# Kernel tuning notes

Measured on AMD Instinct MI355X. Metric: run time of the kernel, lower is better.

## Reference

```python
import jax, jax.numpy as jnp
import numpy as np

B, S, D, H = 2, 2048, 1024, 16
HD = D // H

def setup_inputs() -> dict:
    key = jax.random.key(0)
    ks = jax.random.split(key, 9)
    scale = 1.0 / np.sqrt(D)
    return {
        "query": jax.random.normal(ks[0], (B, S, D), jnp.float32),
        "key":   jax.random.normal(ks[1], (B, S, D), jnp.float32),
        "value": jax.random.normal(ks[2], (B, S, D), jnp.float32),
        "Wq_w": jax.random.normal(ks[3], (D, D), jnp.float32) * scale,
        "Wq_b": jax.random.normal(ks[4], (D,), jnp.float32) * scale,
        "Wk_w": jax.random.normal(ks[5], (D, D), jnp.float32) * scale,
        "Wk_b": jax.random.normal(ks[6], (D,), jnp.float32) * scale,
        "Wv_w": jax.random.normal(ks[7], (D, D), jnp.float32) * scale,
        "Wv_b": jax.random.normal(ks[8], (D,), jnp.float32) * scale,
    }

def reference(query, key, value, Wq_w, Wq_b, Wk_w, Wk_b, Wv_w, Wv_b):
    b, s, d = query.shape
    # torch Linear: y = x @ W.T + b
    Q = query @ Wq_w.T + Wq_b
    K = key   @ Wk_w.T + Wk_b
    V = value @ Wv_w.T + Wv_b
    # [B, H, S, HD]
    Q = Q.reshape(b, -1, H, HD).transpose(0, 2, 1, 3)
    K = K.reshape(b, -1, H, HD).transpose(0, 2, 1, 3)
    V = V.reshape(b, -1, H, HD).transpose(0, 2, 1, 3)
    scores = jnp.einsum("bhqd,bhkd->bhqk", Q, K) / jnp.sqrt(jnp.float32(HD))
    attn = jax.nn.softmax(scores, axis=-1)
    context = jnp.einsum("bhqk,bhkd->bhqd", attn, V)  # [B,H,S,HD]
    attn_output = context.transpose(0, 2, 1, 3).reshape(b, -1, H * HD)  # [B,S,D]
    return (context, attn_output)
```

## Files before the change

### kernel.cpp

```cpp
#include <hip/hip_runtime.h>
#include <hip/hip_bf16.h>

constexpr int Bb = 2, Ss = 2048, Dd = 1024, Hh = 16, HD = 64;
constexpr int Mrows = Bb * Ss;
constexpr float QSCALE = 0.125f * 1.44269504088896f;
constexpr size_t CTX_ELEMS = (size_t)Bb * Hh * Ss * HD;

typedef __attribute__((ext_vector_type(8)))  short        short8;
typedef __attribute__((ext_vector_type(4)))  float        floatx4;
typedef __attribute__((ext_vector_type(16))) float        floatx16;
typedef __attribute__((ext_vector_type(4)))  unsigned int uintx4;
typedef __attribute__((ext_vector_type(8)))  __bf16       bf16x8;

#define DEVI __device__ __forceinline__

DEVI unsigned short f2bf(float f) {
  union { float f; unsigned u; } x; x.f = f;
  return (unsigned short)((x.u + 0x7fffu + ((x.u >> 16) & 1u)) >> 16);
}
DEVI float fexp2(float x) {
#if __has_builtin(__builtin_amdgcn_exp2f)
  return __builtin_amdgcn_exp2f(x);
#else
  return __expf(x * 0.6931471805599453f);
#endif
}

constexpr size_t XE = (size_t)Mrows * Dd;
constexpr size_t WE = (size_t)Dd * Dd;
constexpr size_t OFF_W = 3 * XE;
constexpr size_t OFF_O = 3 * XE + 3 * WE;
constexpr size_t WS_NEED = (OFF_O + 3 * XE) * 2;

__global__ __launch_bounds__(256) void convert_bf16(
    const float* __restrict__ q, const float* __restrict__ k, const float* __restrict__ v,
    const float* __restrict__ wq, const float* __restrict__ wk, const float* __restrict__ wv,
    unsigned short* __restrict__ dst)
{
  const int sel = blockIdx.y;
  const float* src; size_t n, off;
  switch (sel) {
    case 0:  src = q;  n = XE; off = 0;            break;
    case 1:  src = k;  n = XE; off = XE;           break;
    case 2:  src = v;  n = XE; off = 2 * XE;       break;
    case 3:  src = wq; n = WE; off = OFF_W;        break;
    case 4:  src = wk; n = WE; off = OFF_W + WE;   break;
    default: src = wv; n = WE; off = OFF_W + 2*WE; break;
  }
  unsigned short* d = dst + off;
  const size_t stride = (size_t)gridDim.x * blockDim.x;
  for (size_t i = (size_t)blockIdx.x * blockDim.x + threadIdx.x; i < n / 8; i += stride) {
    const floatx4 a = *(const floatx4*)(src + i * 8);
    const floatx4 b = *(const floatx4*)(src + i * 8 + 4);
    short8 o;
    #pragma unroll
    for (int j = 0; j < 4; ++j) { o[j] = (short)f2bf(a[j]); o[4 + j] = (short)f2bf(b[j]); }
    *(short8*)(d + i * 8) = o;
  }
}

template<bool SWAP>
DEVI void store_out(floatx4 (&acc)[4][4], const float* __restrict__ bias,
                    unsigned short* __restrict__ out, float oscale,
                    int bm, int bn, int wm, int wn, int lrow, int lg)
{
  if constexpr (!SWAP) {
    #pragma unroll
    for (int ni = 0; ni < 4; ++ni) {
      const int gcol = bn * 128 + wn + ni * 16 + lrow;
      const float bval = bias[gcol];
      const int h = gcol >> 6, hd = gcol & 63;
      #pragma unroll
      for (int mi = 0; mi < 4; ++mi)
        #pragma unroll
        for (int r = 0; r < 4; ++r) {
          const int grow = bm * 128 + wm + mi * 16 + lg * 4 + r;
          const int b = grow >> 11, s = grow & 2047;
          out[(((size_t)(b * Hh + h) * Ss + s) << 6) + hd] = f2bf((acc[mi][ni][r] + bval) * oscale);
        }
    }
  } else {
    #pragma unroll
    for (int ni = 0; ni < 4; ++ni)
      #pragma unroll
      for (int r = 0; r < 4; ++r) {
        const int n = bn * 128 + wn + ni * 16 + lg * 4 + r;
        const float bval = bias[n];
        #pragma unroll
        for (int mi = 0; mi < 4; ++mi) {
          const int m = bm * 128 + wm + mi * 16 + lrow;
          out[(size_t)n * Mrows + m] = f2bf(acc[mi][ni][r] + bval);
        }
      }
  }
}

DEVI void gload16(const unsigned short* g, unsigned short* l) {
  __builtin_amdgcn_global_load_lds(
      (const __attribute__((address_space(1))) unsigned int*)g,
      (__attribute__((address_space(3))) unsigned int*)l, 16, 0, 0);
}

template<bool SWAP>
DEVI void gemm_core_bf16(const unsigned short* __restrict__ X,
                         const unsigned short* __restrict__ W,
                         const float* __restrict__ bias,
                         unsigned short* __restrict__ out, float oscale,
                         unsigned short* As, unsigned short* Bs, int bm, int bn)
{
  const int t = threadIdx.x, wid = t >> 6, lane = t & 63;
  const int lrow = lane & 15, lg = lane >> 4;
  const int wm = (wid >> 1) * 64, wn = (wid & 1) * 64;

  const int srow = lane >> 3;
  const int gch  = (lane & 7) ^ srow;
  const unsigned short* gA = X + (size_t)(bm * 128 + wid * 32 + srow) * Dd + gch * 8;
  const unsigned short* gB = W + (size_t)(bn * 128 + wid * 32 + srow) * Dd + gch * 8;
  unsigned short* lA = As + wid * 4 * 512;
  unsigned short* lB = Bs + wid * 4 * 512;

  floatx4 acc[4][4];
  #pragma unroll
  for (int i = 0; i < 4; ++i)
    #pragma unroll
    for (int j = 0; j < 4; ++j) acc[i][j] = 0.0f;

  for (int k0 = 0; k0 < Dd; k0 += 64) {
    __syncthreads();
    #pragma unroll
    for (int j = 0; j < 4; ++j) {
      gload16(gA + (size_t)j * 8 * Dd + k0, lA + j * 512);
      gload16(gB + (size_t)j * 8 * Dd + k0, lB + j * 512);
    }
    __syncthreads();

    #pragma unroll
    for (int kf = 0; kf < 2; ++kf) {
      bf16x8 af[4], bf[4];
      #pragma unroll
      for (int mi = 0; mi < 4; ++mi) {
        const int row = wm + mi * 16 + lrow;
        const int ch  = ((kf << 2) | lg) ^ (lrow & 7);
        af[mi] = __builtin_bit_cast(bf16x8, *(const short8*)&As[row * 64 + (ch << 3)]);
      }
      #pragma unroll
      for (int ni = 0; ni < 4; ++ni) {
        const int row = wn + ni * 16 + lrow;
        const int ch  = ((kf << 2) | lg) ^ (lrow & 7);
        bf[ni] = __builtin_bit_cast(bf16x8, *(const short8*)&Bs[row * 64 + (ch << 3)]);
      }
      #pragma unroll
      for (int mi = 0; mi < 4; ++mi)
        #pragma unroll
        for (int ni = 0; ni < 4; ++ni) {
          if constexpr (SWAP)
            acc[mi][ni] = __builtin_amdgcn_mfma_f32_16x16x32_bf16(bf[ni], af[mi], acc[mi][ni], 0, 0, 0);
          else
            acc[mi][ni] = __builtin_amdgcn_mfma_f32_16x16x32_bf16(af[mi], bf[ni], acc[mi][ni], 0, 0, 0);
        }
    }
  }
  store_out<SWAP>(acc, bias, out, oscale, bm, bn, wm, wn, lrow, lg);
}

__global__ __launch_bounds__(256, 3) void qkv_gemm_bf16(
    const unsigned short* __restrict__ ws,
    const float* __restrict__ bq, const float* __restrict__ bk, const float* __restrict__ bv,
    unsigned short* __restrict__ outbase)
{
  __shared__ __align__(16) unsigned short As[128 * 64];
  __shared__ __align__(16) unsigned short Bs[128 * 64];

  const int id  = blockIdx.y * 256 + blockIdx.x;
  const int swz = (id & 7) * 96 + (id >> 3);
  const int sel = swz >> 8;
  const int bx  = swz & 255;
  const int bm = bx >> 3, bn = bx & 7;

  const unsigned short* X = ws + (size_t)sel * XE;
  const unsigned short* W = ws + OFF_W + (size_t)sel * WE;
  const float* bias = sel == 0 ? bq : sel == 1 ? bk : bv;
  unsigned short* out = outbase + (size_t)sel * XE;

  if (sel == 2) gemm_core_bf16<true >(X, W, bias, out, 1.0f,   As, Bs, bm, bn);
  else          gemm_core_bf16<false>(X, W, bias, out, sel == 0 ? QSCALE : 1.0f, As, Bs, bm, bn);
}

constexpr int APAD = 40;

template<bool SWAP>
DEVI void gemm_core_f32(const float* __restrict__ X, const float* __restrict__ W,
                        const float* __restrict__ bias, unsigned short* __restrict__ out,
                        float oscale, unsigned short* As, unsigned short* Bs, int bm, int bn)
{
  const int t = threadIdx.x, wid = t >> 6, lane = t & 63;
  const int lrow = lane & 15, lg = lane >> 4;
  const int wm = (wid >> 1) * 64, wn = (wid & 1) * 64;

  floatx4 acc[4][4];
  #pragma unroll
  for (int i = 0; i < 4; ++i)
    #pragma unroll
    for (int j = 0; j < 4; ++j) acc[i][j] = 0.0f;

  for (int k0 = 0; k0 < Dd; k0 += 32) {
    __syncthreads();
    #pragma unroll
    for (int half = 0; half < 2; ++half) {
      const int cidx = t + half * 256;
      const int r = cidx >> 2, c = cidx & 3;
      {
        const float* ga = X + (size_t)(bm * 128 + r) * Dd + k0 + c * 8;
        const floatx4 x0 = *(const floatx4*)ga;
        const floatx4 x1 = *(const floatx4*)(ga + 4);
        short8 va;
        #pragma unroll
        for (int j = 0; j < 4; ++j) { va[j] = (short)f2bf(x0[j]); va[4+j] = (short)f2bf(x1[j]); }
        *(short8*)&As[r * APAD + c * 8] = va;
      }
      {
        const float* gb = W + (size_t)(bn * 128 + r) * Dd + k0 + c * 8;
        const floatx4 x0 = *(const floatx4*)gb;
        const floatx4 x1 = *(const floatx4*)(gb + 4);
        short8 vb;
        #pragma unroll
        for (int j = 0; j < 4; ++j) { vb[j] = (short)f2bf(x0[j]); vb[4+j] = (short)f2bf(x1[j]); }
        *(short8*)&Bs[r * APAD + c * 8] = vb;
      }
    }
    __syncthreads();

    bf16x8 af[4], bf[4];
    #pragma unroll
    for (int mi = 0; mi < 4; ++mi)
      af[mi] = __builtin_bit_cast(bf16x8, *(const short8*)&As[(wm + mi * 16 + lrow) * APAD + lg * 8]);
    #pragma unroll
    for (int ni = 0; ni < 4; ++ni)
      bf[ni] = __builtin_bit_cast(bf16x8, *(const short8*)&Bs[(wn + ni * 16 + lrow) * APAD + lg * 8]);

    #pragma unroll
    for (int mi = 0; mi < 4; ++mi)
      #pragma unroll
      for (int ni = 0; ni < 4; ++ni) {
        if constexpr (SWAP)
          acc[mi][ni] = __builtin_amdgcn_mfma_f32_16x16x32_bf16(bf[ni], af[mi], acc[mi][ni], 0, 0, 0);
        else
          acc[mi][ni] = __builtin_amdgcn_mfma_f32_16x16x32_bf16(af[mi], bf[ni], acc[mi][ni], 0, 0, 0);
      }
  }
  store_out<SWAP>(acc, bias, out, oscale, bm, bn, wm, wn, lrow, lg);
}

__global__ __launch_bounds__(256, 2) void qkv_gemm_f32(
    const float* __restrict__ q, const float* __restrict__ k, const float* __restrict__ v,
    const float* __restrict__ wq, const float* __restrict__ wk, const float* __restrict__ wv,
    const float* __restrict__ bq, const float* __restrict__ bk, const float* __restrict__ bv,
    unsigned short* __restrict__ outbase)
{
  __shared__ __align__(16) unsigned short As[128 * APAD];
  __shared__ __align__(16) unsigned short Bs[128 * APAD];

  const int id  = blockIdx.y * 256 + blockIdx.x;
  const int swz = (id & 7) * 96 + (id >> 3);
  const int sel = swz >> 8;
  const int bx  = swz & 255;
  const int bm = bx >> 3, bn = bx & 7;

  const float* X = sel == 0 ? q : sel == 1 ? k : v;
  const float* W = sel == 0 ? wq : sel == 1 ? wk : wv;
  const float* bias = sel == 0 ? bq : sel == 1 ? bk : bv;
  unsigned short* out = outbase + (size_t)sel * XE;

  if (sel == 2) gemm_core_f32<true >(X, W, bias, out, 1.0f, As, Bs, bm, bn);
  else          gemm_core_f32<false>(X, W, bias, out, sel == 0 ? QSCALE : 1.0f, As, Bs, bm, bn);
}

__global__ __launch_bounds__(256, 2) void attn_fwd(
    const unsigned short* __restrict__ Qw, const unsigned short* __restrict__ Kw,
    const unsigned short* __restrict__ Vw, float* __restrict__ out)
{
  __shared__ __align__(16) unsigned short Ks[2][64 * 64];
  __shared__ __align__(16) unsigned short Vt[2][64 * 64];

  const int id  = blockIdx.y * 16 + blockIdx.x;
  const int swz = (id & 7) * 64 + (id >> 3);
  const int qb  = swz & 15, bh = swz >> 4;
  const int b   = bh >> 4, h = bh & 15;

  const int t = threadIdx.x, wid = t >> 6, lane = t & 63;
  const int l31 = lane & 31, hi = lane >> 5;
  const unsigned short* Qb = Qw + (size_t)bh * (Ss * HD);
  const unsigned short* Kb = Kw + (size_t)bh * (Ss * HD);
  const unsigned short* Vg = Vw + (size_t)(h * 64) * Mrows + b * Ss;
  const int q0 = qb * 128 + wid * 32;

  bf16x8 qf[4];
  #pragma unroll
  for (int hs = 0; hs < 4; ++hs)
    qf[hs] = __builtin_bit_cast(bf16x8,
        *(const short8*)(Qb + (size_t)(q0 + l31) * 64 + hs * 16 + hi * 8));

  floatx16 ctx[2], lsum;
  #pragma unroll
  for (int nb = 0; nb < 2; ++nb) ctx[nb] = 0.0f;
  lsum = 0.0f;

  short8 ones_s;
  #pragma unroll
  for (int j = 0; j < 8; ++j) ones_s[j] = (short)0x3F80;
  const bf16x8 ones = __builtin_bit_cast(bf16x8, ones_s);

  const int rl = lane >> 3;
  const int cs = (lane & 7) ^ rl;
  auto stage = [&](int kv0, int buf) {
    #pragma unroll
    for (int i = 0; i < 2; ++i) {
      const int row = wid * 16 + i * 8 + rl;
      gload16(Kb + (size_t)(kv0 + row) * 64 + cs * 8, &Ks[buf][(wid * 16 + i * 8) * 64]);
      gload16(Vg + (size_t)row * Mrows + kv0 + cs * 8, &Vt[buf][(wid * 16 + i * 8) * 64]);
    }
  };

  stage(0, 0);

  for (int it = 0; it < Ss / 64; ++it) {
    const int cur = it & 1;
    __syncthreads();
    if (it + 1 < Ss / 64) stage((it + 1) * 64, cur ^ 1);

    floatx16 s[2];
    s[0] = 0.0f; s[1] = 0.0f;
    __builtin_amdgcn_s_setprio(1);
    #pragma unroll
    for (int kvb = 0; kvb < 2; ++kvb)
      #pragma unroll
      for (int hs = 0; hs < 4; ++hs) {
        const int ch = ((hs << 1) | hi) ^ (l31 & 7);
        const bf16x8 kf = __builtin_bit_cast(bf16x8,
            *(const short8*)&Ks[cur][(kvb * 32 + l31) * 64 + (ch << 3)]);
        s[kvb] = __builtin_amdgcn_mfma_f32_32x32x16_bf16(kf, qf[hs], s[kvb], 0, 0, 0);
      }
    __builtin_amdgcn_s_setprio(0);

    #pragma unroll
    for (int kvb = 0; kvb < 2; ++kvb) {
      float p[16];
      #pragma unroll
      for (int r = 0; r < 16; ++r) p[r] = fexp2(s[kvb][r]);
      unsigned int c[8];
      #pragma unroll
      for (int i = 0; i < 8; ++i)
        asm("v_cvt_pk_bf16_f32 %0, %1, %2" : "=v"(c[i]) : "v"(p[2 * i]), "v"(p[2 * i + 1]));

      #pragma unroll
      for (int ks2 = 0; ks2 < 2; ++ks2) {
        unsigned int w0 = c[4 * ks2 + 0], w2 = c[4 * ks2 + 2];
        unsigned int w1 = c[4 * ks2 + 1], w3 = c[4 * ks2 + 3];
        asm("v_permlane32_swap_b32 %0, %1" : "+v"(w0), "+v"(w2));
        asm("v_permlane32_swap_b32 %0, %1" : "+v"(w1), "+v"(w3));
        uintx4 paw; paw[0] = w0; paw[1] = w1; paw[2] = w2; paw[3] = w3;
        const bf16x8 pa = __builtin_bit_cast(bf16x8, paw);

        const int ks = kvb * 2 + ks2;
        __builtin_amdgcn_s_setprio(1);
        lsum = __builtin_amdgcn_mfma_f32_32x32x16_bf16(pa, ones, lsum, 0, 0, 0);
        #pragma unroll
        for (int nb = 0; nb < 2; ++nb) {
          const int ch = ((ks << 1) | hi) ^ (l31 & 7);
          const bf16x8 vf = __builtin_bit_cast(bf16x8,
              *(const short8*)&Vt[cur][(nb * 32 + l31) * 64 + (ch << 3)]);
          ctx[nb] = __builtin_amdgcn_mfma_f32_32x32x16_bf16(pa, vf, ctx[nb], 0, 0, 0);
        }
        __builtin_amdgcn_s_setprio(0);
      }
    }
  }

  #pragma unroll
  for (int r = 0; r < 16; ++r) {
    const float inv = 1.0f / lsum[r];
    const int qrow = q0 + (r & 3) + 8 * (r >> 2) + 4 * hi;
    #pragma unroll
    for (int nb = 0; nb < 2; ++nb) {
      const int hd = nb * 32 + l31;
      const float val = ctx[nb][r] * inv;
      out[((size_t)bh * Ss + qrow) * 64 + hd] = val;
      out[CTX_ELEMS + (((size_t)(b * Ss + qrow)) << 10) + (h << 6) + hd] = val;
    }
  }
}

extern "C" void kernel_launch(void* const* d_in, const int* in_sizes, int n_in,
                              void* d_out, int out_size, void* d_ws, size_t ws_size,
                              hipStream_t stream) {
  const float* q  = (const float*)d_in[0];
  const float* k  = (const float*)d_in[1];
  const float* v  = (const float*)d_in[2];
  const float* wq = (const float*)d_in[3];
  const float* bq = (const float*)d_in[4];
  const float* wk = (const float*)d_in[5];
  const float* bk = (const float*)d_in[6];
  const float* wv = (const float*)d_in[7];
  const float* bv = (const float*)d_in[8];
  unsigned short* ws = (unsigned short*)d_ws;
  float* out = (float*)d_out;

  if (ws_size >= WS_NEED) {
    convert_bf16<<<dim3(256, 6), 256, 0, stream>>>(q, k, v, wq, wk, wv, ws);
    qkv_gemm_bf16<<<dim3(256, 3), 256, 0, stream>>>(ws, bq, bk, bv, ws + OFF_O);
    attn_fwd<<<dim3(16, 32), 256, 0, stream>>>(ws + OFF_O, ws + OFF_O + XE, ws + OFF_O + 2 * XE, out);
  } else {
    qkv_gemm_f32<<<dim3(256, 3), 256, 0, stream>>>(q, k, v, wq, wk, wv, bq, bk, bv, ws);
    attn_fwd<<<dim3(16, 32), 256, 0, stream>>>(ws, ws + XE, ws + 2 * XE, out);
  }
}
```

Before: 92.97 us.

## Load K/V tiles directly from global into registers, dropping LDS staging

New measurement: 164.2 us. 76.6% more time.

```diff
diff --git a/kernel.cpp b/kernel.cpp
--- a/kernel.cpp
+++ b/kernel.cpp
@@ -275,13 +275,12 @@
   else          gemm_core_f32<false>(X, W, bias, out, sel == 0 ? QSCALE : 1.0f, As, Bs, bm, bn);
 }
 
+constexpr int NT = Ss / 64;
+
 __global__ __launch_bounds__(256, 2) void attn_fwd(
     const unsigned short* __restrict__ Qw, const unsigned short* __restrict__ Kw,
     const unsigned short* __restrict__ Vw, float* __restrict__ out)
 {
-  __shared__ __align__(16) unsigned short Ks[2][64 * 64];
-  __shared__ __align__(16) unsigned short Vt[2][64 * 64];
-
   const int id  = blockIdx.y * 16 + blockIdx.x;
   const int swz = (id & 7) * 64 + (id >> 3);
   const int qb  = swz & 15, bh = swz >> 4;
@@ -289,10 +288,11 @@
 
   const int t = threadIdx.x, wid = t >> 6, lane = t & 63;
   const int l31 = lane & 31, hi = lane >> 5;
-  const unsigned short* Qb = Qw + (size_t)bh * (Ss * HD);
-  const unsigned short* Kb = Kw + (size_t)bh * (Ss * HD);
-  const unsigned short* Vg = Vw + (size_t)(h * 64) * Mrows + b * Ss;
   const int q0 = qb * 128 + wid * 32;
+
+  const unsigned short* Qb  = Qw + (size_t)bh * (Ss * HD);
+  const unsigned short* KbL = Kw + (size_t)bh * (Ss * HD) + (size_t)l31 * 64 + hi * 8;
+  const unsigned short* VbL = Vw + (size_t)(h * 64 + l31) * Mrows + b * Ss + hi * 8;
 
   bf16x8 qf[4];
   #pragma unroll
@@ -301,32 +301,36 @@
         *(const short8*)(Qb + (size_t)(q0 + l31) * 64 + hs * 16 + hi * 8));
 
   floatx16 ctx[2], lsum;
-  #pragma unroll
-  for (int nb = 0; nb < 2; ++nb) ctx[nb] = 0.0f;
-  lsum = 0.0f;
+  ctx[0] = 0.0f; ctx[1] = 0.0f; lsum = 0.0f;
 
   short8 ones_s;
   #pragma unroll
   for (int j = 0; j < 8; ++j) ones_s[j] = (short)0x3F80;
   const bf16x8 ones = __builtin_bit_cast(bf16x8, ones_s);
 
-  const int rl = lane >> 3;
-  const int cs = (lane & 7) ^ rl;
-  auto stage = [&](int kv0, int buf) {
-    #pragma unroll
-    for (int i = 0; i < 2; ++i) {
-      const int row = wid * 16 + i * 8 + rl;
-      gload16(Kb + (size_t)(kv0 + row) * 64 + cs * 8, &Ks[buf][(wid * 16 + i * 8) * 64]);
-      gload16(Vg + (size_t)row * Mrows + kv0 + cs * 8, &Vt[buf][(wid * 16 + i * 8) * 64]);
-    }
+  auto loadK = [&](bf16x8 (&kd)[8], int kv0) {
+    #pragma unroll
+    for (int kvb = 0; kvb < 2; ++kvb)
+      #pragma unroll
+      for (int hs = 0; hs < 4; ++hs)
+        kd[kvb * 4 + hs] = __builtin_bit_cast(bf16x8,
+            *(const short8*)(KbL + (size_t)(kv0 + kvb * 32) * 64 + hs * 16));
   };
-
-  stage(0, 0);
-
-  for (int it = 0; it < Ss / 64; ++it) {
-    const int cur = it & 1;
-    __syncthreads();
-    if (it + 1 < Ss / 64) stage((it + 1) * 64, cur ^ 1);
+  auto loadV = [&](bf16x8 (&vd)[8], int kv0) {
+    #pragma unroll
+    for (int nb = 0; nb < 2; ++nb)
+      #pragma unroll
+      for (int ks = 0; ks < 4; ++ks)
+        vd[nb * 4 + ks] = __builtin_bit_cast(bf16x8,
+            *(const short8*)(VbL + (size_t)(nb * 32) * Mrows + kv0 + ks * 16));
+  };
+
+  auto tile = [&](bf16x8 (&kc)[8], bf16x8 (&kn)[8], int it) {
+    const int kv0 = it * 64;
+    bf16x8 vb[8];
+    loadV(vb, kv0);
+    const int kvn = (it + 1 < NT) ? kv0 + 64 : 0;
+    loadK(kn, kvn);
 
     floatx16 s[2];
     s[0] = 0.0f; s[1] = 0.0f;
@@ -334,12 +338,8 @@
     #pragma unroll
     for (int kvb = 0; kvb < 2; ++kvb)
       #pragma unroll
-      for (int hs = 0; hs < 4; ++hs) {
-        const int ch = ((hs << 1) | hi) ^ (l31 & 7);
-        const bf16x8 kf = __builtin_bit_cast(bf16x8,
-            *(const short8*)&Ks[cur][(kvb * 32 + l31) * 64 + (ch << 3)]);
-        s[kvb] = __builtin_amdgcn_mfma_f32_32x32x16_bf16(kf, qf[hs], s[kvb], 0, 0, 0);
-      }
+      for (int hs = 0; hs < 4; ++hs)
+        s[kvb] = __builtin_amdgcn_mfma_f32_32x32x16_bf16(kc[kvb * 4 + hs], qf[hs], s[kvb], 0, 0, 0);
     __builtin_amdgcn_s_setprio(0);
 
     #pragma unroll
@@ -364,16 +364,18 @@
         const int ks = kvb * 2 + ks2;
         __builtin_amdgcn_s_setprio(1);
         lsum = __builtin_amdgcn_mfma_f32_32x32x16_bf16(pa, ones, lsum, 0, 0, 0);
-        #pragma unroll
-        for (int nb = 0; nb < 2; ++nb) {
-          const int ch = ((ks << 1) | hi) ^ (l31 & 7);
-          const bf16x8 vf = __builtin_bit_cast(bf16x8,
-              *(const short8*)&Vt[cur][(nb * 32 + l31) * 64 + (ch << 3)]);
-          ctx[nb] = __builtin_amdgcn_mfma_f32_32x32x16_bf16(pa, vf, ctx[nb], 0, 0, 0);
-        }
+        ctx[0] = __builtin_amdgcn_mfma_f32_32x32x16_bf16(pa, vb[ks],     ctx[0], 0, 0, 0);
+        ctx[1] = __builtin_amdgcn_mfma_f32_32x32x16_bf16(pa, vb[4 + ks], ctx[1], 0, 0, 0);
         __builtin_amdgcn_s_setprio(0);
       }
     }
+  };
+
+  bf16x8 kA[8], kB[8];
+  loadK(kA, 0);
+  for (int it = 0; it < NT; it += 2) {
+    tile(kA, kB, it);
+    tile(kB, kA, it + 1);
   }
 
   #pragma unroll
```

## Software-pipeline attention loop to overlap next tile's QK softmax with current PV

Applied to the files above, without the earlier changes.

Measured after the change: 93.28 us. Within noise of the previous version (+0.3%).

```diff
diff --git a/kernel.cpp b/kernel.cpp
--- a/kernel.cpp
+++ b/kernel.cpp
@@ -275,6 +275,8 @@
   else          gemm_core_f32<false>(X, W, bias, out, sel == 0 ? QSCALE : 1.0f, As, Bs, bm, bn);
 }
 
+constexpr int NT = Ss / 64;
+
 __global__ __launch_bounds__(256, 2) void attn_fwd(
     const unsigned short* __restrict__ Qw, const unsigned short* __restrict__ Kw,
     const unsigned short* __restrict__ Vw, float* __restrict__ out)
@@ -301,9 +303,7 @@
         *(const short8*)(Qb + (size_t)(q0 + l31) * 64 + hs * 16 + hi * 8));
 
   floatx16 ctx[2], lsum;
-  #pragma unroll
-  for (int nb = 0; nb < 2; ++nb) ctx[nb] = 0.0f;
-  lsum = 0.0f;
+  ctx[0] = 0.0f; ctx[1] = 0.0f; lsum = 0.0f;
 
   short8 ones_s;
   #pragma unroll
@@ -312,7 +312,8 @@
 
   const int rl = lane >> 3;
   const int cs = (lane & 7) ^ rl;
-  auto stage = [&](int kv0, int buf) {
+  auto stage = [&](int T) {
+    const int kv0 = T * 64, buf = T & 1;
     #pragma unroll
     for (int i = 0; i < 2; ++i) {
       const int row = wid * 16 + i * 8 + rl;
@@ -321,13 +322,8 @@
     }
   };
 
-  stage(0, 0);
-
-  for (int it = 0; it < Ss / 64; ++it) {
-    const int cur = it & 1;
-    __syncthreads();
-    if (it + 1 < Ss / 64) stage((it + 1) * 64, cur ^ 1);
-
+  auto qk_soft = [&](int T, uintx4 (&pa)[4]) {
+    const int cur = T & 1;
     floatx16 s[2];
     s[0] = 0.0f; s[1] = 0.0f;
     __builtin_amdgcn_s_setprio(1);
@@ -351,7 +347,6 @@
       #pragma unroll
       for (int i = 0; i < 8; ++i)
         asm("v_cvt_pk_bf16_f32 %0, %1, %2" : "=v"(c[i]) : "v"(p[2 * i]), "v"(p[2 * i + 1]));
-
       #pragma unroll
       for (int ks2 = 0; ks2 < 2; ++ks2) {
         unsigned int w0 = c[4 * ks2 + 0], w2 = c[4 * ks2 + 2];
@@ -359,21 +354,46 @@
         asm("v_permlane32_swap_b32 %0, %1" : "+v"(w0), "+v"(w2));
         asm("v_permlane32_swap_b32 %0, %1" : "+v"(w1), "+v"(w3));
         uintx4 paw; paw[0] = w0; paw[1] = w1; paw[2] = w2; paw[3] = w3;
-        const bf16x8 pa = __builtin_bit_cast(bf16x8, paw);
-
-        const int ks = kvb * 2 + ks2;
-        __builtin_amdgcn_s_setprio(1);
-        lsum = __builtin_amdgcn_mfma_f32_32x32x16_bf16(pa, ones, lsum, 0, 0, 0);
-        #pragma unroll
-        for (int nb = 0; nb < 2; ++nb) {
-          const int ch = ((ks << 1) | hi) ^ (l31 & 7);
-          const bf16x8 vf = __builtin_bit_cast(bf16x8,
-              *(const short8*)&Vt[cur][(nb * 32 + l31) * 64 + (ch << 3)]);
-          ctx[nb] = __builtin_amdgcn_mfma_f32_32x32x16_bf16(pa, vf, ctx[nb], 0, 0, 0);
-        }
-        __builtin_amdgcn_s_setprio(0);
-      }
-    }
+        pa[kvb * 2 + ks2] = paw;
+      }
+    }
+  };
+
+  auto body = [&](int t_, uintx4 (&paC)[4], uintx4 (&paN)[4]) {
+    const int cur = t_ & 1;
+    bf16x8 vb[8];
+    #pragma unroll
+    for (int nb = 0; nb < 2; ++nb)
+      #pragma unroll
+      for (int ks = 0; ks < 4; ++ks) {
+        const int ch = ((ks << 1) | hi) ^ (l31 & 7);
+        vb[nb * 4 + ks] = __builtin_bit_cast(bf16x8,
+            *(const short8*)&Vt[cur][(nb * 32 + l31) * 64 + (ch << 3)]);
+      }
+    __syncthreads();
+    if (t_ + 2 < NT) stage(t_ + 2);
+    if (t_ + 1 < NT) qk_soft(t_ + 1, paN);
+
+    __builtin_amdgcn_s_setprio(1);
+    #pragma unroll
+    for (int ks = 0; ks < 4; ++ks) {
+      const bf16x8 pab = __builtin_bit_cast(bf16x8, paC[ks]);
+      lsum   = __builtin_amdgcn_mfma_f32_32x32x16_bf16(pab, ones,       lsum,   0, 0, 0);
+      ctx[0] = __builtin_amdgcn_mfma_f32_32x32x16_bf16(pab, vb[ks],     ctx[0], 0, 0, 0);
+      ctx[1] = __builtin_amdgcn_mfma_f32_32x32x16_bf16(pab, vb[4 + ks], ctx[1], 0, 0, 0);
+    }
+    __builtin_amdgcn_s_setprio(0);
+  };
+
+  stage(0);
+  stage(1);
+  __syncthreads();
+  uintx4 paA[4], paB[4];
+  qk_soft(0, paA);
+
+  for (int it = 0; it < NT; it += 2) {
+    body(it,     paA, paB);
+    body(it + 1, paB, paA);
   }
 
   #pragma unroll
```

## Split attention KV range in halves with combine kernel, replace MFMA row-sum

Applied to the files above, without the earlier changes.

New measurement: 100.6 us. 8.2% more time.

```diff
diff --git a/kernel.cpp b/kernel.cpp
--- a/kernel.cpp
+++ b/kernel.cpp
@@ -31,6 +31,9 @@
 constexpr size_t OFF_W = 3 * XE;
 constexpr size_t OFF_O = 3 * XE + 3 * WE;
 constexpr size_t WS_NEED = (OFF_O + 3 * XE) * 2;
+constexpr size_t P0_E = 0;
+constexpr size_t LA_E = 8388608;
+constexpr size_t LB_E = 8912896;
 
 __global__ __launch_bounds__(256) void convert_bf16(
     const float* __restrict__ q, const float* __restrict__ k, const float* __restrict__ v,
@@ -275,17 +278,32 @@
   else          gemm_core_f32<false>(X, W, bias, out, sel == 0 ? QSCALE : 1.0f, As, Bs, bm, bn);
 }
 
-__global__ __launch_bounds__(256, 2) void attn_fwd(
+template<bool SPLIT>
+__global__ __launch_bounds__(256, 4) void attn_fwd(
     const unsigned short* __restrict__ Qw, const unsigned short* __restrict__ Kw,
-    const unsigned short* __restrict__ Vw, float* __restrict__ out)
+    const unsigned short* __restrict__ Vw,
+    float* __restrict__ p0, float* __restrict__ la,
+    float* __restrict__ p1, float* __restrict__ lb,
+    float* __restrict__ out)
 {
   __shared__ __align__(16) unsigned short Ks[2][64 * 64];
   __shared__ __align__(16) unsigned short Vt[2][64 * 64];
-
-  const int id  = blockIdx.y * 16 + blockIdx.x;
-  const int swz = (id & 7) * 64 + (id >> 3);
-  const int qb  = swz & 15, bh = swz >> 4;
-  const int b   = bh >> 4, h = bh & 15;
+  __shared__ float Ld[4][32];
+
+  int kh, qb, bh, ntiles;
+  if constexpr (SPLIT) {
+    const int id  = blockIdx.y * 32 + blockIdx.x;
+    const int swz = (id & 7) * 128 + (id >> 3);
+    kh = swz & 1; qb = (swz >> 1) & 15; bh = swz >> 5;
+    ntiles = 16;
+  } else {
+    const int id  = blockIdx.y * 16 + blockIdx.x;
+    const int swz = (id & 7) * 64 + (id >> 3);
+    kh = 0; qb = swz & 15; bh = swz >> 4;
+    ntiles = 32;
+  }
+  const int kvbase = kh * 1024;
+  const int b = bh >> 4, h = bh & 15;
 
   const int t = threadIdx.x, wid = t >> 6, lane = t & 63;
   const int l31 = lane & 31, hi = lane >> 5;
@@ -300,19 +318,14 @@
     qf[hs] = __builtin_bit_cast(bf16x8,
         *(const short8*)(Qb + (size_t)(q0 + l31) * 64 + hs * 16 + hi * 8));
 
-  floatx16 ctx[2], lsum;
-  #pragma unroll
-  for (int nb = 0; nb < 2; ++nb) ctx[nb] = 0.0f;
-  lsum = 0.0f;
-
-  short8 ones_s;
-  #pragma unroll
-  for (int j = 0; j < 8; ++j) ones_s[j] = (short)0x3F80;
-  const bf16x8 ones = __builtin_bit_cast(bf16x8, ones_s);
+  floatx16 ctx[2];
+  ctx[0] = 0.0f; ctx[1] = 0.0f;
+  float lsumv = 0.0f;
 
   const int rl = lane >> 3;
   const int cs = (lane & 7) ^ rl;
-  auto stage = [&](int kv0, int buf) {
+  auto stage = [&](int T) {
+    const int kv0 = kvbase + T * 64, buf = T & 1;
     #pragma unroll
     for (int i = 0; i < 2; ++i) {
       const int row = wid * 16 + i * 8 + rl;
@@ -321,32 +334,29 @@
     }
   };
 
-  stage(0, 0);
-
-  for (int it = 0; it < Ss / 64; ++it) {
+  stage(0);
+
+  for (int it = 0; it < ntiles; ++it) {
     const int cur = it & 1;
     __syncthreads();
-    if (it + 1 < Ss / 64) stage((it + 1) * 64, cur ^ 1);
-
-    floatx16 s[2];
-    s[0] = 0.0f; s[1] = 0.0f;
-    __builtin_amdgcn_s_setprio(1);
-    #pragma unroll
-    for (int kvb = 0; kvb < 2; ++kvb)
+    if (it + 1 < ntiles) stage(it + 1);
+
+    #pragma unroll
+    for (int kvb = 0; kvb < 2; ++kvb) {
+      floatx16 s = 0.0f;
+      __builtin_amdgcn_s_setprio(1);
       #pragma unroll
       for (int hs = 0; hs < 4; ++hs) {
         const int ch = ((hs << 1) | hi) ^ (l31 & 7);
         const bf16x8 kf = __builtin_bit_cast(bf16x8,
             *(const short8*)&Ks[cur][(kvb * 32 + l31) * 64 + (ch << 3)]);
-        s[kvb] = __builtin_amdgcn_mfma_f32_32x32x16_bf16(kf, qf[hs], s[kvb], 0, 0, 0);
-      }
-    __builtin_amdgcn_s_setprio(0);
-
-    #pragma unroll
-    for (int kvb = 0; kvb < 2; ++kvb) {
+        s = __builtin_amdgcn_mfma_f32_32x32x16_bf16(kf, qf[hs], s, 0, 0, 0);
+      }
+      __builtin_amdgcn_s_setprio(0);
+
       float p[16];
       #pragma unroll
-      for (int r = 0; r < 16; ++r) p[r] = fexp2(s[kvb][r]);
+      for (int r = 0; r < 16; ++r) { p[r] = fexp2(s[r]); lsumv += p[r]; }
       unsigned int c[8];
       #pragma unroll
       for (int i = 0; i < 8; ++i)
@@ -363,7 +373,6 @@
 
         const int ks = kvb * 2 + ks2;
         __builtin_amdgcn_s_setprio(1);
-        lsum = __builtin_amdgcn_mfma_f32_32x32x16_bf16(pa, ones, lsum, 0, 0, 0);
         #pragma unroll
         for (int nb = 0; nb < 2; ++nb) {
           const int ch = ((ks << 1) | hi) ^ (l31 & 7);
@@ -376,18 +385,56 @@
     }
   }
 
+  float sa = lsumv, sb = lsumv;
+  asm("v_permlane32_swap_b32 %0, %1" : "+v"(sa), "+v"(sb));
+  const float tot = lsumv + (hi ? sa : sb);
+
+  if constexpr (SPLIT) {
+    float* lx = kh ? lb : la;
+    if (hi == 0) lx[bh * Ss + q0 + l31] = tot;
+    float* dst = kh ? p1 : p0;
+    #pragma unroll
+    for (int r = 0; r < 16; ++r) {
+      const int qrow = q0 + (r & 3) + 8 * (r >> 2) + 4 * hi;
+      #pragma unroll
+      for (int nb = 0; nb < 2; ++nb)
+        dst[((size_t)bh * Ss + qrow) * 64 + nb * 32 + l31] = ctx[nb][r];
+    }
+  } else {
+    if (hi == 0) Ld[wid][l31] = tot;
+    #pragma unroll
+    for (int r = 0; r < 16; ++r) {
+      const int wr = (r & 3) + 8 * (r >> 2) + 4 * hi;
+      const float inv = 1.0f / Ld[wid][wr];
+      const int qrow = q0 + wr;
+      #pragma unroll
+      for (int nb = 0; nb < 2; ++nb) {
+        const int hd = nb * 32 + l31;
+        const float val = ctx[nb][r] * inv;
+        out[((size_t)bh * Ss + qrow) * 64 + hd] = val;
+        out[CTX_ELEMS + (((size_t)(b * Ss + qrow)) << 10) + (h << 6) + hd] = val;
+      }
+    }
+  }
+}
+
+__global__ __launch_bounds__(256) void combine_halves(
+    const float* __restrict__ p0, const float* __restrict__ la,
+    const float* __restrict__ lb, float* __restrict__ out)
+{
+  const size_t i4   = (size_t)blockIdx.x * 256 + threadIdx.x;
+  const size_t base = i4 * 4;
+  const floatx4 a = *(const floatx4*)(p0 + base);
+  const floatx4 c = *(const floatx4*)(out + base);
+  const int q  = (int)(base >> 6);
+  const float inv = 1.0f / (la[q] + lb[q]);
+  floatx4 v;
   #pragma unroll
-  for (int r = 0; r < 16; ++r) {
-    const float inv = 1.0f / lsum[r];
-    const int qrow = q0 + (r & 3) + 8 * (r >> 2) + 4 * hi;
-    #pragma unroll
-    for (int nb = 0; nb < 2; ++nb) {
-      const int hd = nb * 32 + l31;
-      const float val = ctx[nb][r] * inv;
-      out[((size_t)bh * Ss + qrow) * 64 + hd] = val;
-      out[CTX_ELEMS + (((size_t)(b * Ss + qrow)) << 10) + (h << 6) + hd] = val;
-    }
-  }
+  for (int j = 0; j < 4; ++j) v[j] = (a[j] + c[j]) * inv;
+  *(floatx4*)(out + base) = v;
+  const int bh = q >> 11, s = q & 2047, hd = (int)(base & 63);
+  const int b = bh >> 4, h = bh & 15;
+  *(floatx4*)(out + CTX_ELEMS + (((size_t)(b * Ss + s)) << 10) + (h << 6) + hd) = v;
 }
 
 extern "C" void kernel_launch(void* const* d_in, const int* in_sizes, int n_in,
@@ -408,9 +455,15 @@
   if (ws_size >= WS_NEED) {
     convert_bf16<<<dim3(256, 6), 256, 0, stream>>>(q, k, v, wq, wk, wv, ws);
     qkv_gemm_bf16<<<dim3(256, 3), 256, 0, stream>>>(ws, bq, bk, bv, ws + OFF_O);
-    attn_fwd<<<dim3(16, 32), 256, 0, stream>>>(ws + OFF_O, ws + OFF_O + XE, ws + OFF_O + 2 * XE, out);
+    float* P0 = (float*)(ws + P0_E);
+    float* LA = (float*)(ws + LA_E);
+    float* LB = (float*)(ws + LB_E);
+    attn_fwd<true><<<dim3(32, 32), 256, 0, stream>>>(
+        ws + OFF_O, ws + OFF_O + XE, ws + OFF_O + 2 * XE, P0, LA, out, LB, out);
+    combine_halves<<<(int)(CTX_ELEMS / 1024), 256, 0, stream>>>(P0, LA, LB, out);
   } else {
     qkv_gemm_f32<<<dim3(256, 3), 256, 0, stream>>>(q, k, v, wq, wk, wv, bq, bk, bv, ws);
-    attn_fwd<<<dim3(16, 32), 256, 0, stream>>>(ws, ws + XE, ws + 2 * XE, out);
-  }
-}
+    attn_fwd<false><<<dim3(16, 32), 256, 0, stream>>>(
+        ws, ws + XE, ws + 2 * XE, nullptr, nullptr, nullptr, nullptr, out);
+  }
+}
```
